# Optimization experiments

Hardware: AMD Instinct MI355X
Metric: run time of the kernel (lower is better)

The kernel has to match this reference:

```python
import jax, jax.numpy as jnp
import numpy as np

EPSILON = 1e-4  # ReEig clamp threshold (init kwarg)


def setup_inputs() -> dict:
    key = jax.random.key(0)
    B, N = 8192, 64
    A = jax.random.normal(key, (B, N, N), dtype=jnp.float32)
    # eigh requires symmetric input; symmetrize like a covariance-style SPD input
    X = 0.5 * (A + jnp.swapaxes(A, -1, -2))
    return {"X": X}


def reference(X) -> jnp.ndarray:
    # D, V = eigh(X); clamp eigenvalues at epsilon; reconstruct V diag(D) V^T
    D, V = jnp.linalg.eigh(X)                 # D: [B,N], V: [B,N,N]
    D = jnp.maximum(D, EPSILON)
    # (V * D[..., None, :]) @ V^T  == V @ diag(D) @ V^T, without materializing diag
    return jnp.einsum("bik,bk,bjk->bij", V, D, V)
```

## Files before the change

### kernel.cpp

```cpp
#include <hip/hip_runtime.h>
#include <hip/hip_bf16.h>


typedef float  f32x4  __attribute__((ext_vector_type(4)));
typedef short  short8 __attribute__((ext_vector_type(8)));

constexpr float EPS_  = 1e-4f;
constexpr int   ITERS = 12;
constexpr int   GROW  = 8;
constexpr int   ONE_LO = 5, ONE_HI = 10;
constexpr int   LDH   = 72;
constexpr int   PLANE = 64 * LDH;
constexpr int   WAVE_S = 2 * PLANE;

struct Frag { short8 hi, lo; };

__device__ __forceinline__ unsigned short bf_hi(float x) {
    return __builtin_bit_cast(unsigned short, __float2bfloat16(x));
}
__device__ __forceinline__ float bf_f(unsigned short h) {
    return __uint_as_float((unsigned)h << 16);
}
__device__ __forceinline__ Frag pack3(const float e[8]) {
    Frag f;
#pragma unroll
    for (int j = 0; j < 8; ++j) {
        const unsigned short h = bf_hi(e[j]);
        f.hi[j] = (short)h;
        f.lo[j] = (short)bf_hi(e[j] - bf_f(h));
    }
    return f;
}
__device__ __forceinline__ f32x4 mfma_bf(short8 a, short8 b, f32x4 c) {
    return __builtin_amdgcn_mfma_f32_16x16x32_bf16(a, b, c, 0, 0, 0);
}
__device__ __forceinline__ f32x4 mfma3(const Frag& a, const Frag& b, f32x4 c) {
    c = mfma_bf(a.hi, b.hi, c);
    c = mfma_bf(a.hi, b.lo, c);
    c = mfma_bf(a.lo, b.hi, c);
    return c;
}

__device__ __forceinline__ void stHL(short* Hhi, short* Hlo, bool lo,
                                     int c, int h4, int i, int j, f32x4 v) {
    const int row = 16 * j + c;
    const int col = (16 * i + 4 * h4) ^ (row & 24);
    const int idx = row * LDH + col;
    unsigned short h0 = bf_hi(v[0]), h1 = bf_hi(v[1]), h2 = bf_hi(v[2]), h3 = bf_hi(v[3]);
    uint2 u;
    u.x = ((unsigned)h1 << 16) | h0;
    u.y = ((unsigned)h3 << 16) | h2;
    *reinterpret_cast<uint2*>(Hhi + idx) = u;
    if (lo) {
        unsigned short l0 = bf_hi(v[0] - bf_f(h0)), l1 = bf_hi(v[1] - bf_f(h1));
        unsigned short l2 = bf_hi(v[2] - bf_f(h2)), l3 = bf_hi(v[3] - bf_f(h3));
        uint2 w;
        w.x = ((unsigned)l1 << 16) | l0;
        w.y = ((unsigned)l3 << 16) | l2;
        *reinterpret_cast<uint2*>(Hlo + idx) = w;
    }
}
__device__ __forceinline__ short8 rdP(const short* H, int c, int h4, int t, int S) {
    const int row = 16 * t + c;
    const int col = (32 * S + 8 * h4) ^ (row & 24);
    return *reinterpret_cast<const short8*>(H + row * LDH + col);
}
__device__ __forceinline__ void load_row8(const float* src, int c, int h4,
                                          int t, int S, float e[8]) {
    const int row = 16 * t + c;
    const float* rp = src + row * 64 + 32 * S + 8 * h4;
    const float4 a = *reinterpret_cast<const float4*>(rp);
    const float4 b = *reinterpret_cast<const float4*>(rp + 4);
    e[0]=a.x; e[1]=a.y; e[2]=a.z; e[3]=a.w;
    e[4]=b.x; e[5]=b.y; e[6]=b.z; e[7]=b.w;
    const int dj = row - (32 * S + 8 * h4);
#pragma unroll
    for (int j = 0; j < 8; ++j) if (j == dj) e[j] -= EPS_;
}
__device__ __forceinline__ void zeroD(f32x4 D[4][4]) {
#pragma unroll
    for (int i = 0; i < 4; ++i)
#pragma unroll
    for (int j = 0; j < 4; ++j) D[i][j] = f32x4{0.f, 0.f, 0.f, 0.f};
}

__global__ __launch_bounds__(256, 2) void reeig_mx(const float* __restrict__ in,
                                                   float* __restrict__ out,
                                                   int* __restrict__ flags) {
    __shared__ __align__(16) short lds4[4 * WAVE_S];

    const int lane = threadIdx.x & 63;
    const int wave = threadIdx.x >> 6;
    const int c    = lane & 15;
    const int h4   = lane >> 4;
    short* Hhi = &lds4[wave * WAVE_S];
    short* Hlo = Hhi + PLANE;

    const long mat = (long)blockIdx.x * 4 + wave;
    const float* __restrict__ src = in  + mat * 4096;
    float*       __restrict__ dst = out + mat * 4096;

    Frag xf[2][4];
    float fro = 0.f;
#pragma unroll
    for (int S = 0; S < 2; ++S)
#pragma unroll
    for (int t = 0; t < 4; ++t) {
        float e[8];
        load_row8(src, c, h4, t, S, e);
#pragma unroll
        for (int j = 0; j < 8; ++j) fro = fmaf(e[j], e[j], fro);
        xf[S][t] = pack3(e);
    }
#pragma unroll
    for (int m = 1; m < 64; m <<= 1) fro += __shfl_xor(fro, m, 64);
    const float invF = rsqrtf(fro);

    float s_acc = 0.f;
    f32x4 D[4][4];

    for (int it = 0; it < ITERS; ++it) {
        const bool three = (it < ONE_LO) || (it >= ONE_HI);
        const bool g1    = !three || (it == ONE_HI);
        const bool xlo0  = (it == ONE_HI);
        const bool xlo_st = three && (it != ONE_LO - 1);
        float c1 = (it < GROW) ? 2.25f    : 1.5f;
        float c3 = (it < GROW) ? -1.6875f : -0.5f;
        if (it == 0) { c1 *= invF; c3 *= invF * invF * invF; }
        if (it == 1) {
            float s = s_acc;
#pragma unroll
            for (int m = 1; m < 64; m <<= 1) s += __shfl_xor(s, m, 64);
            const float mu = sqrtf(sqrtf(s)) * invF;
            const float xm = fminf(mu, 0.6666667f);
            const float fv = 2.25f * xm - 1.6875f * xm * xm * xm;
            const float im = 0.98f / fv;
            c1 *= im; c3 *= im * im * im;
        }
        c1 *= 0.5f; c3 *= 0.5f;

        zeroD(D);
#pragma unroll
        for (int S = 0; S < 2; ++S)
#pragma unroll
        for (int i = 0; i < 4; ++i)
#pragma unroll
        for (int j = 0; j < 4; ++j) {
            if (g1) D[i][j] = mfma_bf(xf[S][i].hi, xf[S][j].hi, D[i][j]);
            else    D[i][j] = mfma3 (xf[S][i],    xf[S][j],    D[i][j]);
        }
        if (it == 0) {
#pragma unroll
            for (int i = 0; i < 4; ++i)
#pragma unroll
            for (int j = 0; j < 4; ++j)
#pragma unroll
            for (int r = 0; r < 4; ++r) s_acc = fmaf(D[i][j][r], D[i][j][r], s_acc);
        }

#pragma unroll
        for (int i = 0; i < 4; ++i)
#pragma unroll
        for (int j = 0; j < 4; ++j) {
            f32x4 v;
#pragma unroll
            for (int r = 0; r < 4; ++r) {
                v[r] = c3 * D[i][j][r];
                if (i == j && c == 4 * h4 + r) v[r] += c1;
            }
            stHL(Hhi, Hlo, three, c, h4, i, j, v);
        }

        zeroD(D);
#pragma unroll
        for (int S = 0; S < 2; ++S) {
            Frag wf[4];
#pragma unroll
            for (int t = 0; t < 4; ++t) {
                wf[t].hi = rdP(Hhi, c, h4, t, S);
                wf[t].lo = three ? rdP(Hlo, c, h4, t, S) : short8{0,0,0,0,0,0,0,0};
            }
#pragma unroll
            for (int i = 0; i < 4; ++i)
#pragma unroll
            for (int j = 0; j < 4; ++j) {
                if (three) {
                    D[i][j] = mfma_bf(xf[S][i].hi, wf[j].hi, D[i][j]);
                    D[i][j] = mfma_bf(xf[S][i].hi, wf[j].lo, D[i][j]);
                    if (!xlo0) D[i][j] = mfma_bf(xf[S][i].lo, wf[j].hi, D[i][j]);
                    D[i][j] = mfma_bf(wf[i].hi, xf[S][j].hi, D[i][j]);
                    D[i][j] = mfma_bf(wf[i].lo, xf[S][j].hi, D[i][j]);
                    if (!xlo0) D[i][j] = mfma_bf(wf[i].hi, xf[S][j].lo, D[i][j]);
                } else {
                    D[i][j] = mfma_bf(xf[S][i].hi, wf[j].hi, D[i][j]);
                    D[i][j] = mfma_bf(wf[i].hi, xf[S][j].hi, D[i][j]);
                }
            }
        }

#pragma unroll
        for (int i = 0; i < 4; ++i)
#pragma unroll
        for (int j = 0; j < 4; ++j) stHL(Hhi, Hlo, xlo_st, c, h4, i, j, D[i][j]);
#pragma unroll
        for (int S = 0; S < 2; ++S)
#pragma unroll
        for (int t = 0; t < 4; ++t) {
            xf[S][t].hi = rdP(Hhi, c, h4, t, S);
            xf[S][t].lo = xlo_st ? rdP(Hlo, c, h4, t, S) : short8{0,0,0,0,0,0,0,0};
        }
    }

    zeroD(D);
#pragma unroll
    for (int S = 0; S < 2; ++S)
#pragma unroll
    for (int i = 0; i < 4; ++i)
#pragma unroll
    for (int j = 0; j < 4; ++j) D[i][j] = mfma_bf(xf[S][i].hi, xf[S][j].hi, D[i][j]);
    float trc = 0.f;
    if (h4 == (c >> 2)) {
        const int r = c - 4 * h4;
#pragma unroll
        for (int i = 0; i < 4; ++i) trc += D[i][i][r];
    }
#pragma unroll
    for (int m = 1; m < 64; m <<= 1) trc += __shfl_xor(trc, m, 64);
    const float trdev = trc - 64.f;
    const bool bad = !(trdev > -4.5f && trdev < 0.9f);

    zeroD(D);
#pragma unroll
    for (int S = 0; S < 2; ++S) {
        Frag b4[4];
#pragma unroll
        for (int t = 0; t < 4; ++t) {
            float e[8]; load_row8(src, c, h4, t, S, e); b4[t] = pack3(e);
        }
#pragma unroll
        for (int i = 0; i < 4; ++i)
#pragma unroll
        for (int j = 0; j < 4; ++j) {
            D[i][j] = mfma3(b4[i], xf[S][j], D[i][j]);
            D[i][j] = mfma3(xf[S][i], b4[j], D[i][j]);
        }
    }

#pragma unroll
    for (int i = 0; i < 4; ++i)
#pragma unroll
    for (int j = 0; j < 4; ++j)
#pragma unroll
    for (int r = 0; r < 4; ++r) {
        const int p = 16 * i + 4 * h4 + r;
        const int q = 16 * j + c;
        const float bval = src[p * 64 + q] - ((p == q) ? EPS_ : 0.f);
        dst[p * 64 + q] = 0.25f * D[i][j][r] + 0.5f * bval + ((p == q) ? EPS_ : 0.f);
    }

    if (lane == 0) flags[mat] = bad ? 1 : 0;
}

constexpr int FB_LD = 68;

__device__ __forceinline__ void fb_mm64(const float* __restrict__ A,
                                        const float* __restrict__ Bm,
                                        int ti, int tj, float acc[4][4]) {
#pragma unroll
    for (int r = 0; r < 4; ++r)
#pragma unroll
        for (int cc = 0; cc < 4; ++cc) acc[r][cc] = 0.f;
#pragma unroll 4
    for (int k = 0; k < 64; ++k) {
        const float4 a = *reinterpret_cast<const float4*>(&A [k * FB_LD + 4 * ti]);
        const float4 b = *reinterpret_cast<const float4*>(&Bm[k * FB_LD + 4 * tj]);
        const float ar[4] = {a.x, a.y, a.z, a.w};
        const float br[4] = {b.x, b.y, b.z, b.w};
#pragma unroll
        for (int r = 0; r < 4; ++r)
#pragma unroll
            for (int cc = 0; cc < 4; ++cc)
                acc[r][cc] = fmaf(ar[r], br[cc], acc[r][cc]);
    }
}

__global__ __launch_bounds__(256) void reeig_fb(const float* __restrict__ in,
                                                float* __restrict__ out,
                                                const int* __restrict__ flags) {
    if (flags && flags[blockIdx.x] == 0) return;

    __shared__ __align__(16) float Bs[64 * FB_LD];
    __shared__ __align__(16) float Xs[64 * FB_LD];
    __shared__ __align__(16) float Ws[64 * FB_LD];
    __shared__ float red[4];

    const int tid = threadIdx.x;
    const int tj  = tid & 15;
    const int ti  = tid >> 4;
    const size_t base = (size_t)blockIdx.x * 4096;
    const float* __restrict__ src = in + base;
    float* __restrict__ dst = out + base;

    float4 v4[4];
    float frob = 0.f;
#pragma unroll
    for (int q = 0; q < 4; ++q) {
        const int idx4 = tid + 256 * q;
        const int lin  = idx4 << 2;
        const int r    = lin >> 6;
        const int c    = lin & 63;
        float4 v = reinterpret_cast<const float4*>(src)[idx4];
        const int d = r - c;
        v.x -= (d == 0) ? EPS_ : 0.f;
        v.y -= (d == 1) ? EPS_ : 0.f;
        v.z -= (d == 2) ? EPS_ : 0.f;
        v.w -= (d == 3) ? EPS_ : 0.f;
        v4[q] = v;
        frob += v.x * v.x + v.y * v.y + v.z * v.z + v.w * v.w;
        *reinterpret_cast<float4*>(&Bs[r * FB_LD + c]) = v;
    }
#pragma unroll
    for (int off = 32; off > 0; off >>= 1) frob += __shfl_down(frob, off);
    if ((tid & 63) == 0) red[tid >> 6] = frob;
    __syncthreads();
    const float tot = red[0] + red[1] + red[2] + red[3];
    const float inv = (tot > 0.f) ? rsqrtf(tot) : 0.f;

#pragma unroll
    for (int q = 0; q < 4; ++q) {
        const int idx4 = tid + 256 * q;
        const int lin  = idx4 << 2;
        const int r    = lin >> 6;
        const int c    = lin & 63;
        float4 v = v4[q];
        v.x *= inv; v.y *= inv; v.z *= inv; v.w *= inv;
        *reinterpret_cast<float4*>(&Xs[r * FB_LD + c]) = v;
    }
    __syncthreads();

    float acc[4][4];
    for (int it = 0; it < 14; ++it) {
        const bool  g  = (it < 9);
        const float c1 = g ? 2.25f    : 1.5f;
        const float c3 = g ? -1.6875f : -0.5f;

        fb_mm64(Xs, Xs, ti, tj, acc);
#pragma unroll
        for (int r = 0; r < 4; ++r) {
            const int i = 4 * ti + r;
            float4 w;
            w.x = c3 * acc[r][0] + ((i == 4 * tj + 0) ? c1 : 0.f);
            w.y = c3 * acc[r][1] + ((i == 4 * tj + 1) ? c1 : 0.f);
            w.z = c3 * acc[r][2] + ((i == 4 * tj + 2) ? c1 : 0.f);
            w.w = c3 * acc[r][3] + ((i == 4 * tj + 3) ? c1 : 0.f);
            *reinterpret_cast<float4*>(&Ws[i * FB_LD + 4 * tj]) = w;
        }
        __syncthreads();

        fb_mm64(Xs, Ws, ti, tj, acc);
        __syncthreads();
#pragma unroll
        for (int r = 0; r < 4; ++r) {
            const int i = 4 * ti + r;
            float4 x;
            x.x = acc[r][0]; x.y = acc[r][1]; x.z = acc[r][2]; x.w = acc[r][3];
            *reinterpret_cast<float4*>(&Xs[i * FB_LD + 4 * tj]) = x;
        }
        __syncthreads();
    }

    fb_mm64(Bs, Xs, ti, tj, acc);
#pragma unroll
    for (int r = 0; r < 4; ++r) {
        const int i = 4 * ti + r;
        float4 o;
        o.x = 0.5f * (acc[r][0] + Bs[i * FB_LD + 4 * tj + 0]) + ((i == 4 * tj + 0) ? EPS_ : 0.f);
        o.y = 0.5f * (acc[r][1] + Bs[i * FB_LD + 4 * tj + 1]) + ((i == 4 * tj + 1) ? EPS_ : 0.f);
        o.z = 0.5f * (acc[r][2] + Bs[i * FB_LD + 4 * tj + 2]) + ((i == 4 * tj + 2) ? EPS_ : 0.f);
        o.w = 0.5f * (acc[r][3] + Bs[i * FB_LD + 4 * tj + 3]) + ((i == 4 * tj + 3) ? EPS_ : 0.f);
        *reinterpret_cast<float4*>(&dst[i * 64 + 4 * tj]) = o;
    }
}

extern "C" void kernel_launch(void* const* d_in, const int* in_sizes, int n_in,
                              void* d_out, int out_size, void* d_ws, size_t ws_size,
                              hipStream_t stream) {
    const float* X = (const float*)d_in[0];
    float* O = (float*)d_out;
    const int nmat = in_sizes[0] / 4096;
    if (ws_size >= (size_t)nmat * sizeof(int)) {
        int* flags = (int*)d_ws;
        reeig_mx<<<nmat / 4, 256, 0, stream>>>(X, O, flags);
        reeig_fb<<<nmat, 256, 0, stream>>>(X, O, flags);
    } else {
        reeig_fb<<<nmat, 256, 0, stream>>>(X, O, nullptr);
    }
}
```

Baseline: 334.3 us.

## Switch matrix-sign iteration from 16x16x32 to 32x32x16 bf16 MFMA tiles

Reworks the per-wave 64x64 GEMMs in the Newton-Schulz-style iteration to use 32x32x16 MFMA instructions with a 2x2 tile grid instead of a 4x4 grid of 16x16 tiles. Fragment loading, LDS store and read layouts, diagonal-shift handling, trace computation and the output indexing are all remapped to the 32x32 accumulator layout. The aim is fewer MFMA issues and fragment loads per GEMM and better operand reuse. The risk is different register pressure and LDS bank-conflict behavior under the existing swizzle.

```diff
diff --git a/kernel.cpp b/kernel.cpp
--- a/kernel.cpp
+++ b/kernel.cpp
@@ -2,7 +2,7 @@
 #include <hip/hip_bf16.h>
 
 
-typedef float  f32x4  __attribute__((ext_vector_type(4)));
+typedef float  f32x16 __attribute__((ext_vector_type(16)));
 typedef short  short8 __attribute__((ext_vector_type(8)));
 
 constexpr float EPS_  = 1e-4f;
@@ -31,57 +31,67 @@
     }
     return f;
 }
-__device__ __forceinline__ f32x4 mfma_bf(short8 a, short8 b, f32x4 c) {
-    return __builtin_amdgcn_mfma_f32_16x16x32_bf16(a, b, c, 0, 0, 0);
-}
-__device__ __forceinline__ f32x4 mfma3(const Frag& a, const Frag& b, f32x4 c) {
+__device__ __forceinline__ f32x16 mfma_bf(short8 a, short8 b, f32x16 c) {
+    return __builtin_amdgcn_mfma_f32_32x32x16_bf16(a, b, c, 0, 0, 0);
+}
+__device__ __forceinline__ f32x16 mfma3(const Frag& a, const Frag& b, f32x16 c) {
     c = mfma_bf(a.hi, b.hi, c);
     c = mfma_bf(a.hi, b.lo, c);
     c = mfma_bf(a.lo, b.hi, c);
     return c;
 }
 
-__device__ __forceinline__ void stHL(short* Hhi, short* Hlo, bool lo,
-                                     int c, int h4, int i, int j, f32x4 v) {
-    const int row = 16 * j + c;
-    const int col = (16 * i + 4 * h4) ^ (row & 24);
-    const int idx = row * LDH + col;
-    unsigned short h0 = bf_hi(v[0]), h1 = bf_hi(v[1]), h2 = bf_hi(v[2]), h3 = bf_hi(v[3]);
-    uint2 u;
-    u.x = ((unsigned)h1 << 16) | h0;
-    u.y = ((unsigned)h3 << 16) | h2;
-    *reinterpret_cast<uint2*>(Hhi + idx) = u;
-    if (lo) {
-        unsigned short l0 = bf_hi(v[0] - bf_f(h0)), l1 = bf_hi(v[1] - bf_f(h1));
-        unsigned short l2 = bf_hi(v[2] - bf_f(h2)), l3 = bf_hi(v[3] - bf_f(h3));
-        uint2 w;
-        w.x = ((unsigned)l1 << 16) | l0;
-        w.y = ((unsigned)l3 << 16) | l2;
-        *reinterpret_cast<uint2*>(Hlo + idx) = w;
-    }
-}
-__device__ __forceinline__ short8 rdP(const short* H, int c, int h4, int t, int S) {
-    const int row = 16 * t + c;
-    const int col = (32 * S + 8 * h4) ^ (row & 24);
+__device__ __forceinline__ void stHL32(short* Hhi, short* Hlo, bool lo,
+                                       int lo5, int hw, int i, int j,
+                                       const f32x16& v) {
+    const int row  = 32 * j + lo5;
+    const int rsw  = row & 24;
+    const int idx0 = row * LDH;
+#pragma unroll
+    for (int rq = 0; rq < 4; ++rq) {
+        const int cb = (32 * i + 8 * rq + 4 * hw) ^ rsw;
+        const float a0 = v[4*rq+0], a1 = v[4*rq+1], a2 = v[4*rq+2], a3 = v[4*rq+3];
+        const unsigned short h0 = bf_hi(a0), h1 = bf_hi(a1);
+        const unsigned short h2 = bf_hi(a2), h3 = bf_hi(a3);
+        uint2 u;
+        u.x = ((unsigned)h1 << 16) | h0;
+        u.y = ((unsigned)h3 << 16) | h2;
+        *reinterpret_cast<uint2*>(Hhi + idx0 + cb) = u;
+        if (lo) {
+            const unsigned short l0 = bf_hi(a0 - bf_f(h0)), l1 = bf_hi(a1 - bf_f(h1));
+            const unsigned short l2 = bf_hi(a2 - bf_f(h2)), l3 = bf_hi(a3 - bf_f(h3));
+            uint2 w;
+            w.x = ((unsigned)l1 << 16) | l0;
+            w.y = ((unsigned)l3 << 16) | l2;
+            *reinterpret_cast<uint2*>(Hlo + idx0 + cb) = w;
+        }
+    }
+}
+__device__ __forceinline__ short8 rdP32(const short* H, int lo5, int hw, int i, int s) {
+    const int row = 32 * i + lo5;
+    const int col = (16 * s + 8 * hw) ^ (row & 24);
     return *reinterpret_cast<const short8*>(H + row * LDH + col);
 }
-__device__ __forceinline__ void load_row8(const float* src, int c, int h4,
-                                          int t, int S, float e[8]) {
-    const int row = 16 * t + c;
-    const float* rp = src + row * 64 + 32 * S + 8 * h4;
+__device__ __forceinline__ void load_row8_32(const float* src, int lo5, int hw,
+                                             int i, int s, float e[8]) {
+    const int row = 32 * i + lo5;
+    const int c0  = 16 * s + 8 * hw;
+    const float* rp = src + row * 64 + c0;
     const float4 a = *reinterpret_cast<const float4*>(rp);
     const float4 b = *reinterpret_cast<const float4*>(rp + 4);
     e[0]=a.x; e[1]=a.y; e[2]=a.z; e[3]=a.w;
     e[4]=b.x; e[5]=b.y; e[6]=b.z; e[7]=b.w;
-    const int dj = row - (32 * S + 8 * h4);
+    const int dj = row - c0;
 #pragma unroll
     for (int j = 0; j < 8; ++j) if (j == dj) e[j] -= EPS_;
 }
-__device__ __forceinline__ void zeroD(f32x4 D[4][4]) {
-#pragma unroll
-    for (int i = 0; i < 4; ++i)
-#pragma unroll
-    for (int j = 0; j < 4; ++j) D[i][j] = f32x4{0.f, 0.f, 0.f, 0.f};
+__device__ __forceinline__ void zeroD(f32x16 D[2][2]) {
+#pragma unroll
+    for (int i = 0; i < 2; ++i)
+#pragma unroll
+    for (int j = 0; j < 2; ++j)
+#pragma unroll
+    for (int r = 0; r < 16; ++r) D[i][j][r] = 0.f;
 }
 
 __global__ __launch_bounds__(256, 2) void reeig_mx(const float* __restrict__ in,
@@ -91,38 +101,42 @@
 
     const int lane = threadIdx.x & 63;
     const int wave = threadIdx.x >> 6;
-    const int c    = lane & 15;
-    const int h4   = lane >> 4;
+    const int lo5  = lane & 31;
+    const int hw   = lane >> 5;
     short* Hhi = &lds4[wave * WAVE_S];
     short* Hlo = Hhi + PLANE;
+
+    const int  vd     = lo5 - 4 * hw;
+    const bool dvalid = (vd >= 0) && ((vd & 4) == 0);
+    const int  rdiag  = dvalid ? ((vd & 3) + 4 * (vd >> 3)) : 0;
 
     const long mat = (long)blockIdx.x * 4 + wave;
     const float* __restrict__ src = in  + mat * 4096;
     float*       __restrict__ dst = out + mat * 4096;
 
-    Frag xf[2][4];
+    Frag xf[4][2];
     float fro = 0.f;
 #pragma unroll
-    for (int S = 0; S < 2; ++S)
-#pragma unroll
-    for (int t = 0; t < 4; ++t) {
+    for (int s = 0; s < 4; ++s)
+#pragma unroll
+    for (int i = 0; i < 2; ++i) {
         float e[8];
-        load_row8(src, c, h4, t, S, e);
+        load_row8_32(src, lo5, hw, i, s, e);
 #pragma unroll
         for (int j = 0; j < 8; ++j) fro = fmaf(e[j], e[j], fro);
-        xf[S][t] = pack3(e);
+        xf[s][i] = pack3(e);
     }
 #pragma unroll
     for (int m = 1; m < 64; m <<= 1) fro += __shfl_xor(fro, m, 64);
     const float invF = rsqrtf(fro);
 
     float s_acc = 0.f;
-    f32x4 D[4][4];
+    f32x16 D[2][2];
 
     for (int it = 0; it < ITERS; ++it) {
-        const bool three = (it < ONE_LO) || (it >= ONE_HI);
-        const bool g1    = !three || (it == ONE_HI);
-        const bool xlo0  = (it == ONE_HI);
+        const bool three  = (it < ONE_LO) || (it >= ONE_HI);
+        const bool g1     = !three || (it == ONE_HI);
+        const bool xlo0   = (it == ONE_HI);
         const bool xlo_st = three && (it != ONE_LO - 1);
         float c1 = (it < GROW) ? 2.25f    : 1.5f;
         float c3 = (it < GROW) ? -1.6875f : -0.5f;
@@ -141,119 +155,120 @@
 
         zeroD(D);
 #pragma unroll
-        for (int S = 0; S < 2; ++S)
-#pragma unroll
-        for (int i = 0; i < 4; ++i)
-#pragma unroll
-        for (int j = 0; j < 4; ++j) {
-            if (g1) D[i][j] = mfma_bf(xf[S][i].hi, xf[S][j].hi, D[i][j]);
-            else    D[i][j] = mfma3 (xf[S][i],    xf[S][j],    D[i][j]);
+        for (int s = 0; s < 4; ++s)
+#pragma unroll
+        for (int i = 0; i < 2; ++i)
+#pragma unroll
+        for (int j = 0; j < 2; ++j) {
+            if (g1) D[i][j] = mfma_bf(xf[s][i].hi, xf[s][j].hi, D[i][j]);
+            else    D[i][j] = mfma3 (xf[s][i],    xf[s][j],    D[i][j]);
         }
         if (it == 0) {
 #pragma unroll
-            for (int i = 0; i < 4; ++i)
-#pragma unroll
-            for (int j = 0; j < 4; ++j)
-#pragma unroll
-            for (int r = 0; r < 4; ++r) s_acc = fmaf(D[i][j][r], D[i][j][r], s_acc);
-        }
-
-#pragma unroll
-        for (int i = 0; i < 4; ++i)
-#pragma unroll
-        for (int j = 0; j < 4; ++j) {
-            f32x4 v;
-#pragma unroll
-            for (int r = 0; r < 4; ++r) {
-                v[r] = c3 * D[i][j][r];
-                if (i == j && c == 4 * h4 + r) v[r] += c1;
+            for (int i = 0; i < 2; ++i)
+#pragma unroll
+            for (int j = 0; j < 2; ++j)
+#pragma unroll
+            for (int r = 0; r < 16; ++r) s_acc = fmaf(D[i][j][r], D[i][j][r], s_acc);
+        }
+
+#pragma unroll
+        for (int i = 0; i < 2; ++i)
+#pragma unroll
+        for (int j = 0; j < 2; ++j) {
+            f32x16 v;
+#pragma unroll
+            for (int r = 0; r < 16; ++r) {
+                float val = c3 * D[i][j][r];
+                if (i == j && dvalid && r == rdiag) val += c1;
+                v[r] = val;
             }
-            stHL(Hhi, Hlo, three, c, h4, i, j, v);
+            stHL32(Hhi, Hlo, three, lo5, hw, i, j, v);
         }
 
         zeroD(D);
 #pragma unroll
-        for (int S = 0; S < 2; ++S) {
-            Frag wf[4];
-#pragma unroll
-            for (int t = 0; t < 4; ++t) {
-                wf[t].hi = rdP(Hhi, c, h4, t, S);
-                wf[t].lo = three ? rdP(Hlo, c, h4, t, S) : short8{0,0,0,0,0,0,0,0};
+        for (int s = 0; s < 4; ++s) {
+            Frag wf[2];
+#pragma unroll
+            for (int t = 0; t < 2; ++t) {
+                wf[t].hi = rdP32(Hhi, lo5, hw, t, s);
+                wf[t].lo = three ? rdP32(Hlo, lo5, hw, t, s) : short8{0,0,0,0,0,0,0,0};
             }
 #pragma unroll
-            for (int i = 0; i < 4; ++i)
-#pragma unroll
-            for (int j = 0; j < 4; ++j) {
+            for (int i = 0; i < 2; ++i)
+#pragma unroll
+            for (int j = 0; j < 2; ++j) {
                 if (three) {
-                    D[i][j] = mfma_bf(xf[S][i].hi, wf[j].hi, D[i][j]);
-                    D[i][j] = mfma_bf(xf[S][i].hi, wf[j].lo, D[i][j]);
-                    if (!xlo0) D[i][j] = mfma_bf(xf[S][i].lo, wf[j].hi, D[i][j]);
-                    D[i][j] = mfma_bf(wf[i].hi, xf[S][j].hi, D[i][j]);
-                    D[i][j] = mfma_bf(wf[i].lo, xf[S][j].hi, D[i][j]);
-                    if (!xlo0) D[i][j] = mfma_bf(wf[i].hi, xf[S][j].lo, D[i][j]);
+                    D[i][j] = mfma_bf(xf[s][i].hi, wf[j].hi, D[i][j]);
+                    D[i][j] = mfma_bf(xf[s][i].hi, wf[j].lo, D[i][j]);
+                    if (!xlo0) D[i][j] = mfma_bf(xf[s][i].lo, wf[j].hi, D[i][j]);
+                    D[i][j] = mfma_bf(wf[i].hi, xf[s][j].hi, D[i][j]);
+                    D[i][j] = mfma_bf(wf[i].lo, xf[s][j].hi, D[i][j]);
+                    if (!xlo0) D[i][j] = mfma_bf(wf[i].hi, xf[s][j].lo, D[i][j]);
                 } else {
-                    D[i][j] = mfma_bf(xf[S][i].hi, wf[j].hi, D[i][j]);
-                    D[i][j] = mfma_bf(wf[i].hi, xf[S][j].hi, D[i][j]);
+                    D[i][j] = mfma_bf(xf[s][i].hi, wf[j].hi, D[i][j]);
+                    D[i][j] = mfma_bf(wf[i].hi, xf[s][j].hi, D[i][j]);
                 }
             }
         }
 
 #pragma unroll
-        for (int i = 0; i < 4; ++i)
-#pragma unroll
-        for (int j = 0; j < 4; ++j) stHL(Hhi, Hlo, xlo_st, c, h4, i, j, D[i][j]);
-#pragma unroll
-        for (int S = 0; S < 2; ++S)
-#pragma unroll
-        for (int t = 0; t < 4; ++t) {
-            xf[S][t].hi = rdP(Hhi, c, h4, t, S);
-            xf[S][t].lo = xlo_st ? rdP(Hlo, c, h4, t, S) : short8{0,0,0,0,0,0,0,0};
+        for (int i = 0; i < 2; ++i)
+#pragma unroll
+        for (int j = 0; j < 2; ++j) stHL32(Hhi, Hlo, xlo_st, lo5, hw, i, j, D[i][j]);
+#pragma unroll
+        for (int s = 0; s < 4; ++s)
+#pragma unroll
+        for (int i = 0; i < 2; ++i) {
+            xf[s][i].hi = rdP32(Hhi, lo5, hw, i, s);
+            xf[s][i].lo = xlo_st ? rdP32(Hlo, lo5, hw, i, s) : short8{0,0,0,0,0,0,0,0};
         }
     }
 
     zeroD(D);
 #pragma unroll
-    for (int S = 0; S < 2; ++S)
-#pragma unroll
-    for (int i = 0; i < 4; ++i)
-#pragma unroll
-    for (int j = 0; j < 4; ++j) D[i][j] = mfma_bf(xf[S][i].hi, xf[S][j].hi, D[i][j]);
+    for (int s = 0; s < 4; ++s)
+#pragma unroll
+    for (int i = 0; i < 2; ++i)
+#pragma unroll
+    for (int j = 0; j < 2; ++j) D[i][j] = mfma_bf(xf[s][i].hi, xf[s][j].hi, D[i][j]);
     float trc = 0.f;
-    if (h4 == (c >> 2)) {
-        const int r = c - 4 * h4;
-#pragma unroll
-        for (int i = 0; i < 4; ++i) trc += D[i][i][r];
+    if (dvalid) {
+#pragma unroll
+        for (int r = 0; r < 16; ++r)
+            if (r == rdiag) trc = D[0][0][r] + D[1][1][r];
     }
 #pragma unroll
     for (int m = 1; m < 64; m <<= 1) trc += __shfl_xor(trc, m, 64);
     const float trdev = trc - 64.f;
-    const bool bad = !(trdev > -4.5f && trdev < 0.9f);
+    const bool  bad   = !(trdev > -4.5f && trdev < 0.9f);
 
     zeroD(D);
 #pragma unroll
-    for (int S = 0; S < 2; ++S) {
-        Frag b4[4];
-#pragma unroll
-        for (int t = 0; t < 4; ++t) {
-            float e[8]; load_row8(src, c, h4, t, S, e); b4[t] = pack3(e);
-        }
-#pragma unroll
-        for (int i = 0; i < 4; ++i)
-#pragma unroll
-        for (int j = 0; j < 4; ++j) {
-            D[i][j] = mfma3(b4[i], xf[S][j], D[i][j]);
-            D[i][j] = mfma3(xf[S][i], b4[j], D[i][j]);
-        }
-    }
-
-#pragma unroll
-    for (int i = 0; i < 4; ++i)
-#pragma unroll
-    for (int j = 0; j < 4; ++j)
-#pragma unroll
-    for (int r = 0; r < 4; ++r) {
-        const int p = 16 * i + 4 * h4 + r;
-        const int q = 16 * j + c;
+    for (int s = 0; s < 4; ++s) {
+        Frag b4[2];
+#pragma unroll
+        for (int t = 0; t < 2; ++t) {
+            float e[8]; load_row8_32(src, lo5, hw, t, s, e); b4[t] = pack3(e);
+        }
+#pragma unroll
+        for (int i = 0; i < 2; ++i)
+#pragma unroll
+        for (int j = 0; j < 2; ++j) {
+            D[i][j] = mfma3(b4[i], xf[s][j], D[i][j]);
+            D[i][j] = mfma3(xf[s][i], b4[j], D[i][j]);
+        }
+    }
+
+#pragma unroll
+    for (int i = 0; i < 2; ++i)
+#pragma unroll
+    for (int j = 0; j < 2; ++j)
+#pragma unroll
+    for (int r = 0; r < 16; ++r) {
+        const int p = 32 * i + (r & 3) + 8 * (r >> 2) + 4 * hw;
+        const int q = 32 * j + lo5;
         const float bval = src[p * 64 + q] - ((p == q) ? EPS_ : 0.f);
         dst[p * 64 + q] = 0.25f * D[i][j][r] + 0.5f * bval + ((p == q) ? EPS_ : 0.f);
     }
```

Result: slower. 365.7 us (+9.4%).
